# Optimization experiments

Measured on AMD Instinct MI355X. Metric: run time of the kernel, lower is better.

The kernel has to match this reference:

```python
import jax, jax.numpy as jnp
import numpy as np

NEG_SLOPE = 0.2  # PyG GATConv default negative_slope
BN_EPS = 1e-5


def _segment_softmax(logits, seg, num_segments):
    # numerically stable softmax over edges grouped by destination node
    m = jax.ops.segment_max(logits, seg, num_segments=num_segments)
    e = jnp.exp(logits - m[seg])
    s = jax.ops.segment_sum(e, seg, num_segments=num_segments)
    return e / s[seg]


def _gat_conv(x, src, dst, W, a_src, a_dst, bias, heads, d_head, concat):
    N = x.shape[0]
    h = (x @ W).reshape(N, heads, d_head)                      # [N, H, D]
    alpha_src = jnp.einsum('nhd,hd->nh', h, a_src)             # [N, H]
    alpha_dst = jnp.einsum('nhd,hd->nh', h, a_dst)             # [N, H]
    logits = jax.nn.leaky_relu(alpha_src[src] + alpha_dst[dst], NEG_SLOPE)  # [E, H]
    alpha = _segment_softmax(logits, dst, N)                   # [E, H]
    msg = h[src] * alpha[:, :, None]                           # [E, H, D]
    out = jax.ops.segment_sum(msg, dst, num_segments=N)        # [N, H, D]
    out = out.reshape(N, heads * d_head) if concat else out.mean(axis=1)
    return out + bias


def setup_inputs() -> dict:
    key = jax.random.key(0)
    ks = jax.random.split(key, 12)
    N, E = 50000, 800000
    in_dim, hidden, out_dim, heads = 256, 128, 2, 4
    d1 = hidden // heads  # 32
    s = 0.05
    return {
        'x': jax.random.normal(ks[0], (N, in_dim), dtype=jnp.float32),
        'edge_index': jax.random.randint(ks[1], (2, E), 0, N, dtype=jnp.int64),
        'W1': jax.random.normal(ks[2], (in_dim, heads * d1), dtype=jnp.float32) * s,
        'att_src1': jax.random.normal(ks[3], (heads, d1), dtype=jnp.float32) * s,
        'att_dst1': jax.random.normal(ks[4], (heads, d1), dtype=jnp.float32) * s,
        'b1': jnp.zeros((heads * d1,), dtype=jnp.float32),
        'bn_gamma': jnp.ones((hidden,), dtype=jnp.float32),
        'bn_beta': jnp.zeros((hidden,), dtype=jnp.float32),
        'bn_mean': jnp.zeros((hidden,), dtype=jnp.float32),
        'bn_var': jnp.ones((hidden,), dtype=jnp.float32),
        'W2': jax.random.normal(ks[5], (hidden, out_dim), dtype=jnp.float32) * s,
        'att_src2': jax.random.normal(ks[6], (1, out_dim), dtype=jnp.float32) * s,
        'att_dst2': jax.random.normal(ks[7], (1, out_dim), dtype=jnp.float32) * s,
        'b2': jnp.zeros((out_dim,), dtype=jnp.float32),
    }


def reference(x, edge_index, W1, att_src1, att_dst1, b1,
              bn_gamma, bn_beta, bn_mean, bn_var,
              W2, att_src2, att_dst2, b2):
    N = x.shape[0]
    # PyG GATConv adds self-loops by default
    loop = jnp.arange(N, dtype=edge_index.dtype)
    src = jnp.concatenate([edge_index[0], loop])
    dst = jnp.concatenate([edge_index[1], loop])

    heads, d1 = att_src1.shape
    h = _gat_conv(x, src, dst, W1, att_src1, att_dst1, b1, heads, d1, concat=True)
    # BatchNorm1d in eval mode (running stats), then ReLU (dropout is a no-op in eval)
    h = (h - bn_mean) * jax.lax.rsqrt(bn_var + BN_EPS) * bn_gamma + bn_beta
    h = jax.nn.relu(h)
    out = _gat_conv(h, src, dst, W2, att_src2, att_dst2, b2, 1, att_src2.shape[1], concat=False)
    return out
```

## Files before the change

### kernel.cpp

```cpp
#include <hip/hip_runtime.h>
#include <hip/hip_bf16.h>

#define LRELU(x) ((x) > 0.f ? (x) : 0.2f * (x))
#define CAP 96
#define BINCAP 4800

typedef short bf16x8 __attribute__((ext_vector_type(8)));
typedef float f32x4 __attribute__((ext_vector_type(4)));

__device__ __forceinline__ float b2f(unsigned short u) {
  union { unsigned int i; float f; } v;
  v.i = ((unsigned int)u) << 16;
  return v.f;
}
__device__ __forceinline__ unsigned short f2b(float f) {
  unsigned int u = __float_as_uint(f);
  unsigned int r = (u + 0x7fffu + ((u >> 16) & 1u)) >> 16;
  return (unsigned short)r;
}

__global__ __launch_bounds__(256) void prep_w1t_kernel(
    const float* __restrict__ W, unsigned short* __restrict__ w1t) {
  int idx = blockIdx.x * 256 + threadIdx.x;
  int n = idx >> 8, k = idx & 255;
  w1t[idx] = f2b(W[k * 128 + n]);
}

__global__ __launch_bounds__(256) void gemm1_mfma_kernel(
    const float* __restrict__ x, const unsigned short* __restrict__ w1t,
    unsigned short* __restrict__ h1bf, int N) {
  __shared__ unsigned short bsh[128 * 264];

  const int tid = threadIdx.x;
#pragma unroll
  for (int i = 0; i < 16; i++) {
    int idx = (i * 256 + tid) * 8;
    int row = idx >> 8;
    int k = idx & 255;
    *(uint4*)(bsh + row * 264 + k) = *(const uint4*)(w1t + row * 256 + k);
  }
  __syncthreads();

  const int m0 = blockIdx.x * 64 + (tid >> 6) * 16;
  if (m0 >= N) return;
  const int lane = tid & 63;
  const int row = lane & 15;
  const int quad = lane >> 4;

  f32x4 acc[8];
#pragma unroll
  for (int t = 0; t < 8; t++) acc[t] = (f32x4){0.f, 0.f, 0.f, 0.f};

  const float* ap = x + (size_t)(m0 + row) * 256 + quad * 8;
#pragma unroll
  for (int k0 = 0; k0 < 256; k0 += 32) {
    float4 av0 = *(const float4*)(ap + k0);
    float4 av1 = *(const float4*)(ap + k0 + 4);
    float af[8] = {av0.x, av0.y, av0.z, av0.w, av1.x, av1.y, av1.z, av1.w};
    bf16x8 ahi, alo;
#pragma unroll
    for (int j = 0; j < 8; j++) {
      unsigned short h = f2b(af[j]);
      ahi[j] = (short)h;
      alo[j] = (short)f2b(af[j] - b2f(h));
    }
#pragma unroll
    for (int t = 0; t < 8; t++) {
      bf16x8 b = *(const bf16x8*)(bsh + (t * 16 + row) * 264 + k0 + quad * 8);
      acc[t] = __builtin_amdgcn_mfma_f32_16x16x32_bf16(ahi, b, acc[t], 0, 0, 0);
      acc[t] = __builtin_amdgcn_mfma_f32_16x16x32_bf16(alo, b, acc[t], 0, 0, 0);
    }
  }
  unsigned short* op = h1bf + (size_t)(m0 + quad * 4) * 128 + row;
#pragma unroll
  for (int t = 0; t < 8; t++)
#pragma unroll
    for (int r = 0; r < 4; r++)
      op[(size_t)r * 128 + t * 16] = f2b(acc[t][r]);
}

__global__ __launch_bounds__(256) void alpha1_kernel(
    const unsigned short* __restrict__ h1bf, const float* __restrict__ att_s,
    const float* __restrict__ att_d, float* __restrict__ asrc,
    float* __restrict__ adst, int N) {
  int idx = blockIdx.x * 256 + threadIdx.x;
  if (idx >= N * 4) return;
  int n = idx >> 2, h = idx & 3;
  const uint4* hp = (const uint4*)(h1bf + (size_t)n * 128 + h * 32);
  const float4* sp = (const float4*)(att_s + h * 32);
  const float4* dp = (const float4*)(att_d + h * 32);
  float ss = 0.f, sd = 0.f;
#pragma unroll
  for (int i = 0; i < 4; i++) {
    uint4 pv = hp[i];
    unsigned int u[4] = {pv.x, pv.y, pv.z, pv.w};
#pragma unroll
    for (int q = 0; q < 4; q++) {
      float v0 = b2f((unsigned short)(u[q] & 0xffff));
      float v1 = b2f((unsigned short)(u[q] >> 16));
      float4 a = sp[i * 2 + (q >> 1)];
      float4 d = dp[i * 2 + (q >> 1)];
      float a0 = (q & 1) ? a.z : a.x, a1 = (q & 1) ? a.w : a.y;
      float d0 = (q & 1) ? d.z : d.x, d1 = (q & 1) ? d.w : d.y;
      ss += v0 * a0 + v1 * a1;
      sd += v0 * d0 + v1 * d1;
    }
  }
  asrc[idx] = ss;
  adst[idx] = sd;
}

__global__ __launch_bounds__(256) void bin_edges_kernel(
    const int* __restrict__ ei, int E, int* __restrict__ gcnt,
    unsigned int* __restrict__ binned, int nbins) {
  __shared__ int hist[256];
  __shared__ int base[256];
  const int tid = threadIdx.x;
  hist[tid] = 0;
  __syncthreads();
  const int chunk = (E + gridDim.x - 1) / gridDim.x;
  const int e0 = blockIdx.x * chunk;
  const int e1 = min(e0 + chunk, E);
  for (int e = e0 + tid; e < e1; e += 256)
    atomicAdd(&hist[ei[(size_t)E + e] >> 8], 1);
  __syncthreads();
  if (tid < nbins && hist[tid] > 0) base[tid] = atomicAdd(&gcnt[tid], hist[tid]);
  __syncthreads();
  hist[tid] = 0;
  __syncthreads();
  for (int e = e0 + tid; e < e1; e += 256) {
    int s = ei[e];
    int t = ei[(size_t)E + e];
    int b = t >> 8;
    int pos = base[b] + atomicAdd(&hist[b], 1);
    if (pos < BINCAP)
      binned[(size_t)b * BINCAP + pos] = ((unsigned int)t << 16) | (unsigned int)s;
  }
}

__global__ __launch_bounds__(256) void bin_to_buckets_kernel(
    const int* __restrict__ gcnt, const unsigned int* __restrict__ binned,
    int* __restrict__ cnt, unsigned short* __restrict__ buckets, int N) {
  __shared__ unsigned short lbkt[256 * CAP];
  __shared__ int lcnt[256];
  const int b = blockIdx.x;
  const int tid = threadIdx.x;
  lcnt[tid] = 0;
  __syncthreads();
  const int ne = min(gcnt[b], BINCAP);
  const unsigned int* bp = binned + (size_t)b * BINCAP;
  for (int i = tid; i < ne; i += 256) {
    unsigned int p = bp[i];
    int ln = (p >> 16) & 255;
    int pos = atomicAdd(&lcnt[ln], 1);
    if (pos < CAP) lbkt[ln * CAP + pos] = (unsigned short)(p & 0xffff);
  }
  __syncthreads();
  const int n0 = b << 8;
  const int nn = min(256, N - n0);
  if (nn <= 0) return;
  if (tid < nn) cnt[n0 + tid] = lcnt[tid];
  const int total8 = (nn * CAP) >> 3;
  uint4* d4 = (uint4*)(buckets + (size_t)n0 * CAP);
  const uint4* s4 = (const uint4*)lbkt;
  for (int i = tid; i < total8; i += 256) d4[i] = s4[i];
}

__global__ __launch_bounds__(256) void agg1_kernel(
    const int* __restrict__ cnt, const unsigned short* __restrict__ buckets,
    const unsigned short* __restrict__ h1bf, const float* __restrict__ asrc,
    const float* __restrict__ adst, const float* __restrict__ b1,
    const float* __restrict__ gamma, const float* __restrict__ beta,
    const float* __restrict__ mean, const float* __restrict__ var,
    const float* __restrict__ W2, const float* __restrict__ as2,
    const float* __restrict__ ad2, float4* __restrict__ pk, int N) {
  const int t = blockIdx.x * 4 + (threadIdx.x >> 6);
  if (t >= N) return;
  const int l = threadIdx.x & 63;
  const int h = l >> 4;
  const float ad = adst[t * 4 + h];

  float acc0 = 0.f, acc1 = 0.f, den = 0.f;
  const unsigned short* bkt = buckets + (size_t)t * CAP;
  const int deg = min(cnt[t], CAP);
  int j = 0;
  for (; j + 4 <= deg; j += 4) {
    int s0 = bkt[j], s1 = bkt[j + 1];
    int s2 = bkt[j + 2], s3 = bkt[j + 3];
    unsigned int p0 = *(const unsigned int*)(h1bf + (size_t)s0 * 128 + 2 * l);
    unsigned int p1 = *(const unsigned int*)(h1bf + (size_t)s1 * 128 + 2 * l);
    unsigned int p2 = *(const unsigned int*)(h1bf + (size_t)s2 * 128 + 2 * l);
    unsigned int p3 = *(const unsigned int*)(h1bf + (size_t)s3 * 128 + 2 * l);
    float w0 = __expf(LRELU(asrc[s0 * 4 + h] + ad));
    float w1 = __expf(LRELU(asrc[s1 * 4 + h] + ad));
    float w2 = __expf(LRELU(asrc[s2 * 4 + h] + ad));
    float w3 = __expf(LRELU(asrc[s3 * 4 + h] + ad));
    acc0 += w0 * b2f((unsigned short)(p0 & 0xffff)) +
            w1 * b2f((unsigned short)(p1 & 0xffff)) +
            w2 * b2f((unsigned short)(p2 & 0xffff)) +
            w3 * b2f((unsigned short)(p3 & 0xffff));
    acc1 += w0 * b2f((unsigned short)(p0 >> 16)) +
            w1 * b2f((unsigned short)(p1 >> 16)) +
            w2 * b2f((unsigned short)(p2 >> 16)) +
            w3 * b2f((unsigned short)(p3 >> 16));
    den += w0 + w1 + w2 + w3;
  }
  for (; j < deg; j++) {
    int s0 = bkt[j];
    unsigned int p0 = *(const unsigned int*)(h1bf + (size_t)s0 * 128 + 2 * l);
    float w0 = __expf(LRELU(asrc[s0 * 4 + h] + ad));
    acc0 += w0 * b2f((unsigned short)(p0 & 0xffff));
    acc1 += w0 * b2f((unsigned short)(p0 >> 16));
    den += w0;
  }
  {
    unsigned int p0 = *(const unsigned int*)(h1bf + (size_t)t * 128 + 2 * l);
    float w0 = __expf(LRELU(asrc[t * 4 + h] + ad));
    acc0 += w0 * b2f((unsigned short)(p0 & 0xffff));
    acc1 += w0 * b2f((unsigned short)(p0 >> 16));
    den += w0;
  }
  const int c0 = 2 * l;
  float inv = 1.f / den;
  float v0 = acc0 * inv + b1[c0];
  float v1 = acc1 * inv + b1[c0 + 1];
  v0 = (v0 - mean[c0]) * rsqrtf(var[c0] + 1e-5f) * gamma[c0] + beta[c0];
  v1 = (v1 - mean[c0 + 1]) * rsqrtf(var[c0 + 1] + 1e-5f) * gamma[c0 + 1] +
       beta[c0 + 1];
  v0 = v0 > 0.f ? v0 : 0.f;
  v1 = v1 > 0.f ? v1 : 0.f;

  float g0 = v0 * W2[c0 * 2 + 0] + v1 * W2[(c0 + 1) * 2 + 0];
  float g1 = v0 * W2[c0 * 2 + 1] + v1 * W2[(c0 + 1) * 2 + 1];
#pragma unroll
  for (int o = 32; o > 0; o >>= 1) {
    g0 += __shfl_down(g0, o);
    g1 += __shfl_down(g1, o);
  }
  if (l == 0) {
    float4 p;
    p.x = g0;
    p.y = g1;
    p.z = g0 * as2[0] + g1 * as2[1];
    p.w = g0 * ad2[0] + g1 * ad2[1];
    pk[t] = p;
  }
}

__global__ __launch_bounds__(256) void agg2_kernel(
    const int* __restrict__ cnt, const unsigned short* __restrict__ buckets,
    const float4* __restrict__ pk, const float* __restrict__ b2,
    float* __restrict__ out, int N) {
  int t = blockIdx.x * 256 + threadIdx.x;
  if (t >= N) return;
  float4 pt = pk[t];
  const float ad = pt.w;
  float a0 = 0.f, a1 = 0.f, den = 0.f;
  const unsigned short* bkt = buckets + (size_t)t * CAP;
  const int deg = min(cnt[t], CAP);
  int j = 0;
  for (; j + 4 <= deg; j += 4) {
    float4 p0 = pk[bkt[j]];
    float4 p1 = pk[bkt[j + 1]];
    float4 p2 = pk[bkt[j + 2]];
    float4 p3 = pk[bkt[j + 3]];
    float w0 = __expf(LRELU(p0.z + ad));
    float w1 = __expf(LRELU(p1.z + ad));
    float w2 = __expf(LRELU(p2.z + ad));
    float w3 = __expf(LRELU(p3.z + ad));
    a0 += w0 * p0.x + w1 * p1.x + w2 * p2.x + w3 * p3.x;
    a1 += w0 * p0.y + w1 * p1.y + w2 * p2.y + w3 * p3.y;
    den += w0 + w1 + w2 + w3;
  }
  for (; j < deg; j++) {
    float4 p0 = pk[bkt[j]];
    float w0 = __expf(LRELU(p0.z + ad));
    a0 += w0 * p0.x;
    a1 += w0 * p0.y;
    den += w0;
  }
  {
    float w0 = __expf(LRELU(pt.z + ad));
    a0 += w0 * pt.x;
    a1 += w0 * pt.y;
    den += w0;
  }
  float2 o;
  o.x = a0 / den + b2[0];
  o.y = a1 / den + b2[1];
  *(float2*)(out + (size_t)t * 2) = o;
}

extern "C" void kernel_launch(void* const* d_in, const int* in_sizes, int n_in,
                              void* d_out, int out_size, void* d_ws,
                              size_t ws_size, hipStream_t stream) {
  const float* x      = (const float*)d_in[0];
  const int*   ei     = (const int*)d_in[1];
  const float* W1     = (const float*)d_in[2];
  const float* atts1  = (const float*)d_in[3];
  const float* attd1  = (const float*)d_in[4];
  const float* b1     = (const float*)d_in[5];
  const float* gamma  = (const float*)d_in[6];
  const float* beta   = (const float*)d_in[7];
  const float* mean   = (const float*)d_in[8];
  const float* var    = (const float*)d_in[9];
  const float* W2     = (const float*)d_in[10];
  const float* atts2  = (const float*)d_in[11];
  const float* attd2  = (const float*)d_in[12];
  const float* b2     = (const float*)d_in[13];
  float* out = (float*)d_out;

  const int N = in_sizes[0] / 256;
  const int E = in_sizes[1] / 2;
  const int nbins = (N + 255) >> 8;

  char* ws = (char*)d_ws;
  size_t off = 0;
  unsigned short* h1bf = (unsigned short*)(ws + off); off += (size_t)N * 128 * 2;
  float* asrc1 = (float*)(ws + off); off += (size_t)N * 4 * 4;
  float* adst1 = (float*)(ws + off); off += (size_t)N * 4 * 4;
  float4* pk   = (float4*)(ws + off); off += (size_t)N * 16;
  int*   cnt   = (int*)  (ws + off); off += (size_t)N * 4;
  int*   gcnt  = (int*)  (ws + off); off += 256 * 4;
  unsigned short* w1t = (unsigned short*)(ws + off); off += 128 * 256 * 2;
  unsigned short* buckets = (unsigned short*)(ws + off);
  off += (size_t)N * CAP * 2;
  unsigned int* binned = (unsigned int*)(ws + off);
  off += (size_t)nbins * BINCAP * 4;

  hipMemsetAsync(gcnt, 0, 256 * 4, stream);
  bin_edges_kernel<<<512, 256, 0, stream>>>(ei, E, gcnt, binned, nbins);
  bin_to_buckets_kernel<<<nbins, 256, 0, stream>>>(gcnt, binned, cnt, buckets,
                                                   N);

  prep_w1t_kernel<<<128, 256, 0, stream>>>(W1, w1t);
  gemm1_mfma_kernel<<<(N + 63) / 64, 256, 0, stream>>>(x, w1t, h1bf, N);
  alpha1_kernel<<<(N * 4 + 255) / 256, 256, 0, stream>>>(h1bf, atts1, attd1,
                                                         asrc1, adst1, N);
  agg1_kernel<<<(N + 3) / 4, 256, 0, stream>>>(cnt, buckets, h1bf, asrc1,
                                               adst1, b1, gamma, beta, mean,
                                               var, W2, atts2, attd2, pk, N);

  agg2_kernel<<<(N + 255) / 256, 256, 0, stream>>>(cnt, buckets, pk, b2, out,
                                                   N);
}
```

Before: 217.5 us.

## Fuse alpha1 into GEMM epilogue, shrink edge bins, parallelize agg2 per node

Computes layer-1 attention logits inside the MFMA GEMM epilogue from fp32 accumulators using lane shuffles, which removes the separate alpha1 kernel and its re-read of h1. Edge binning now uses 128-node bins instead of 256, giving twice as many bucket blocks and half the shared memory per block. agg2 switches from one thread per node to 16 lanes per node with a shuffle reduction, to spread the gather latency. Alpha is now computed from unrounded fp32 values, so results can differ slightly from before.

```diff
diff --git a/kernel.cpp b/kernel.cpp
--- a/kernel.cpp
+++ b/kernel.cpp
@@ -3,7 +3,8 @@
 
 #define LRELU(x) ((x) > 0.f ? (x) : 0.2f * (x))
 #define CAP 96
-#define BINCAP 4800
+#define BINBITS 7
+#define BINCAP 2600
 
 typedef short bf16x8 __attribute__((ext_vector_type(8)));
 typedef float f32x4 __attribute__((ext_vector_type(4)));
@@ -28,7 +29,9 @@
 
 __global__ __launch_bounds__(256) void gemm1_mfma_kernel(
     const float* __restrict__ x, const unsigned short* __restrict__ w1t,
-    unsigned short* __restrict__ h1bf, int N) {
+    const float* __restrict__ atts, const float* __restrict__ attd,
+    unsigned short* __restrict__ h1bf, float* __restrict__ asrc,
+    float* __restrict__ adst, int N) {
   __shared__ unsigned short bsh[128 * 264];
 
   const int tid = threadIdx.x;
@@ -77,61 +80,67 @@
 #pragma unroll
     for (int r = 0; r < 4; r++)
       op[(size_t)r * 128 + t * 16] = f2b(acc[t][r]);
-}
-
-__global__ __launch_bounds__(256) void alpha1_kernel(
-    const unsigned short* __restrict__ h1bf, const float* __restrict__ att_s,
-    const float* __restrict__ att_d, float* __restrict__ asrc,
-    float* __restrict__ adst, int N) {
-  int idx = blockIdx.x * 256 + threadIdx.x;
-  if (idx >= N * 4) return;
-  int n = idx >> 2, h = idx & 3;
-  const uint4* hp = (const uint4*)(h1bf + (size_t)n * 128 + h * 32);
-  const float4* sp = (const float4*)(att_s + h * 32);
-  const float4* dp = (const float4*)(att_d + h * 32);
-  float ss = 0.f, sd = 0.f;
-#pragma unroll
-  for (int i = 0; i < 4; i++) {
-    uint4 pv = hp[i];
-    unsigned int u[4] = {pv.x, pv.y, pv.z, pv.w};
-#pragma unroll
-    for (int q = 0; q < 4; q++) {
-      float v0 = b2f((unsigned short)(u[q] & 0xffff));
-      float v1 = b2f((unsigned short)(u[q] >> 16));
-      float4 a = sp[i * 2 + (q >> 1)];
-      float4 d = dp[i * 2 + (q >> 1)];
-      float a0 = (q & 1) ? a.z : a.x, a1 = (q & 1) ? a.w : a.y;
-      float d0 = (q & 1) ? d.z : d.x, d1 = (q & 1) ? d.w : d.y;
-      ss += v0 * a0 + v1 * a1;
-      sd += v0 * d0 + v1 * d1;
+
+  float asv[8], adv[8];
+#pragma unroll
+  for (int t = 0; t < 8; t++) {
+    asv[t] = atts[t * 16 + row];
+    adv[t] = attd[t * 16 + row];
+  }
+  float ps[4][4], pd[4][4];
+#pragma unroll
+  for (int h = 0; h < 4; h++)
+#pragma unroll
+    for (int r = 0; r < 4; r++) {
+      ps[h][r] = acc[2 * h][r] * asv[2 * h] + acc[2 * h + 1][r] * asv[2 * h + 1];
+      pd[h][r] = acc[2 * h][r] * adv[2 * h] + acc[2 * h + 1][r] * adv[2 * h + 1];
     }
-  }
-  asrc[idx] = ss;
-  adst[idx] = sd;
+#pragma unroll
+  for (int o = 1; o < 16; o <<= 1) {
+#pragma unroll
+    for (int h = 0; h < 4; h++)
+#pragma unroll
+      for (int r = 0; r < 4; r++) {
+        ps[h][r] += __shfl_xor(ps[h][r], o);
+        pd[h][r] += __shfl_xor(pd[h][r], o);
+      }
+  }
+  if (row == 0) {
+#pragma unroll
+    for (int r = 0; r < 4; r++) {
+      int m = m0 + quad * 4 + r;
+#pragma unroll
+      for (int h = 0; h < 4; h++) {
+        asrc[m * 4 + h] = ps[h][r];
+        adst[m * 4 + h] = pd[h][r];
+      }
+    }
+  }
 }
 
 __global__ __launch_bounds__(256) void bin_edges_kernel(
     const int* __restrict__ ei, int E, int* __restrict__ gcnt,
     unsigned int* __restrict__ binned, int nbins) {
-  __shared__ int hist[256];
-  __shared__ int base[256];
+  __shared__ int hist[512];
+  __shared__ int base[512];
   const int tid = threadIdx.x;
-  hist[tid] = 0;
+  for (int i = tid; i < 512; i += 256) hist[i] = 0;
   __syncthreads();
   const int chunk = (E + gridDim.x - 1) / gridDim.x;
   const int e0 = blockIdx.x * chunk;
   const int e1 = min(e0 + chunk, E);
   for (int e = e0 + tid; e < e1; e += 256)
-    atomicAdd(&hist[ei[(size_t)E + e] >> 8], 1);
-  __syncthreads();
-  if (tid < nbins && hist[tid] > 0) base[tid] = atomicAdd(&gcnt[tid], hist[tid]);
-  __syncthreads();
-  hist[tid] = 0;
+    atomicAdd(&hist[ei[(size_t)E + e] >> BINBITS], 1);
+  __syncthreads();
+  for (int i = tid; i < nbins; i += 256)
+    if (hist[i] > 0) base[i] = atomicAdd(&gcnt[i], hist[i]);
+  __syncthreads();
+  for (int i = tid; i < 512; i += 256) hist[i] = 0;
   __syncthreads();
   for (int e = e0 + tid; e < e1; e += 256) {
     int s = ei[e];
     int t = ei[(size_t)E + e];
-    int b = t >> 8;
+    int b = t >> BINBITS;
     int pos = base[b] + atomicAdd(&hist[b], 1);
     if (pos < BINCAP)
       binned[(size_t)b * BINCAP + pos] = ((unsigned int)t << 16) | (unsigned int)s;
@@ -141,23 +150,23 @@
 __global__ __launch_bounds__(256) void bin_to_buckets_kernel(
     const int* __restrict__ gcnt, const unsigned int* __restrict__ binned,
     int* __restrict__ cnt, unsigned short* __restrict__ buckets, int N) {
-  __shared__ unsigned short lbkt[256 * CAP];
-  __shared__ int lcnt[256];
+  __shared__ unsigned short lbkt[128 * CAP];
+  __shared__ int lcnt[128];
   const int b = blockIdx.x;
   const int tid = threadIdx.x;
-  lcnt[tid] = 0;
+  if (tid < 128) lcnt[tid] = 0;
   __syncthreads();
   const int ne = min(gcnt[b], BINCAP);
   const unsigned int* bp = binned + (size_t)b * BINCAP;
   for (int i = tid; i < ne; i += 256) {
     unsigned int p = bp[i];
-    int ln = (p >> 16) & 255;
+    int ln = (p >> 16) & 127;
     int pos = atomicAdd(&lcnt[ln], 1);
     if (pos < CAP) lbkt[ln * CAP + pos] = (unsigned short)(p & 0xffff);
   }
   __syncthreads();
-  const int n0 = b << 8;
-  const int nn = min(256, N - n0);
+  const int n0 = b << BINBITS;
+  const int nn = min(128, N - n0);
   if (nn <= 0) return;
   if (tid < nn) cnt[n0 + tid] = lcnt[tid];
   const int total8 = (nn * CAP) >> 3;
@@ -251,44 +260,37 @@
     const int* __restrict__ cnt, const unsigned short* __restrict__ buckets,
     const float4* __restrict__ pk, const float* __restrict__ b2,
     float* __restrict__ out, int N) {
-  int t = blockIdx.x * 256 + threadIdx.x;
+  const int t = blockIdx.x * 16 + (threadIdx.x >> 4);
   if (t >= N) return;
+  const int lg = threadIdx.x & 15;
   float4 pt = pk[t];
   const float ad = pt.w;
   float a0 = 0.f, a1 = 0.f, den = 0.f;
   const unsigned short* bkt = buckets + (size_t)t * CAP;
   const int deg = min(cnt[t], CAP);
-  int j = 0;
-  for (; j + 4 <= deg; j += 4) {
-    float4 p0 = pk[bkt[j]];
-    float4 p1 = pk[bkt[j + 1]];
-    float4 p2 = pk[bkt[j + 2]];
-    float4 p3 = pk[bkt[j + 3]];
-    float w0 = __expf(LRELU(p0.z + ad));
-    float w1 = __expf(LRELU(p1.z + ad));
-    float w2 = __expf(LRELU(p2.z + ad));
-    float w3 = __expf(LRELU(p3.z + ad));
-    a0 += w0 * p0.x + w1 * p1.x + w2 * p2.x + w3 * p3.x;
-    a1 += w0 * p0.y + w1 * p1.y + w2 * p2.y + w3 * p3.y;
-    den += w0 + w1 + w2 + w3;
-  }
-  for (; j < deg; j++) {
-    float4 p0 = pk[bkt[j]];
-    float w0 = __expf(LRELU(p0.z + ad));
-    a0 += w0 * p0.x;
-    a1 += w0 * p0.y;
-    den += w0;
-  }
-  {
-    float w0 = __expf(LRELU(pt.z + ad));
-    a0 += w0 * pt.x;
-    a1 += w0 * pt.y;
-    den += w0;
-  }
-  float2 o;
-  o.x = a0 / den + b2[0];
-  o.y = a1 / den + b2[1];
-  *(float2*)(out + (size_t)t * 2) = o;
+  for (int j = lg; j < deg; j += 16) {
+    float4 p = pk[bkt[j]];
+    float w = __expf(LRELU(p.z + ad));
+    a0 += w * p.x;
+    a1 += w * p.y;
+    den += w;
+  }
+#pragma unroll
+  for (int o = 8; o > 0; o >>= 1) {
+    a0 += __shfl_xor(a0, o);
+    a1 += __shfl_xor(a1, o);
+    den += __shfl_xor(den, o);
+  }
+  if (lg == 0) {
+    float w = __expf(LRELU(pt.z + ad));
+    a0 += w * pt.x;
+    a1 += w * pt.y;
+    den += w;
+    float2 o2;
+    o2.x = a0 / den + b2[0];
+    o2.y = a1 / den + b2[1];
+    *(float2*)(out + (size_t)t * 2) = o2;
+  }
 }
 
 extern "C" void kernel_launch(void* const* d_in, const int* in_sizes, int n_in,
@@ -312,7 +314,7 @@
 
   const int N = in_sizes[0] / 256;
   const int E = in_sizes[1] / 2;
-  const int nbins = (N + 255) >> 8;
+  const int nbins = (N + (1 << BINBITS) - 1) >> BINBITS;
 
   char* ws = (char*)d_ws;
   size_t off = 0;
@@ -321,26 +323,24 @@
   float* adst1 = (float*)(ws + off); off += (size_t)N * 4 * 4;
   float4* pk   = (float4*)(ws + off); off += (size_t)N * 16;
   int*   cnt   = (int*)  (ws + off); off += (size_t)N * 4;
-  int*   gcnt  = (int*)  (ws + off); off += 256 * 4;
+  int*   gcnt  = (int*)  (ws + off); off += 512 * 4;
   unsigned short* w1t = (unsigned short*)(ws + off); off += 128 * 256 * 2;
   unsigned short* buckets = (unsigned short*)(ws + off);
   off += (size_t)N * CAP * 2;
   unsigned int* binned = (unsigned int*)(ws + off);
   off += (size_t)nbins * BINCAP * 4;
 
-  hipMemsetAsync(gcnt, 0, 256 * 4, stream);
+  hipMemsetAsync(gcnt, 0, 512 * 4, stream);
   bin_edges_kernel<<<512, 256, 0, stream>>>(ei, E, gcnt, binned, nbins);
   bin_to_buckets_kernel<<<nbins, 256, 0, stream>>>(gcnt, binned, cnt, buckets,
                                                    N);
 
   prep_w1t_kernel<<<128, 256, 0, stream>>>(W1, w1t);
-  gemm1_mfma_kernel<<<(N + 63) / 64, 256, 0, stream>>>(x, w1t, h1bf, N);
-  alpha1_kernel<<<(N * 4 + 255) / 256, 256, 0, stream>>>(h1bf, atts1, attd1,
-                                                         asrc1, adst1, N);
+  gemm1_mfma_kernel<<<(N + 63) / 64, 256, 0, stream>>>(
+      x, w1t, atts1, attd1, h1bf, asrc1, adst1, N);
   agg1_kernel<<<(N + 3) / 4, 256, 0, stream>>>(cnt, buckets, h1bf, asrc1,
                                                adst1, b1, gamma, beta, mean,
                                                var, W2, atts2, attd2, pk, N);
 
-  agg2_kernel<<<(N + 255) / 256, 256, 0, stream>>>(cnt, buckets, pk, b2, out,
-                                                   N);
-}
+  agg2_kernel<<<(N + 15) / 16, 256, 0, stream>>>(cnt, buckets, pk, b2, out, N);
+}
```

Result: faster. 209.1 us (-3.9%).
